# Kernel optimization log

Measured on AMD Instinct MI355X. Metric: run time of the kernel, lower is better.

The kernel has to match this reference:

```python
import jax, jax.numpy as jnp
import numpy as np

T = 2048          # tokens (single causal prefill sequence)
H = 4096          # hidden_size
NH = 32           # num query heads
NKV = 8           # num kv heads (GQA)
HD = H // NH      # head_dim = 128
ROPE_THETA = 500000.0
Q_SIZE = NH * HD
KV_SIZE = NKV * HD


def setup_inputs() -> dict:
    key = jax.random.key(0)
    k1, k2, k3 = jax.random.split(key, 3)
    return {
        "positions": jnp.arange(T, dtype=jnp.int32),
        "hidden_states": jax.random.normal(k1, (T, H), dtype=jnp.float32) * 0.02,
        "w_qkv": jax.random.normal(k2, (H, Q_SIZE + 2 * KV_SIZE), dtype=jnp.float32) * (1.0 / np.sqrt(H)),
        "w_o": jax.random.normal(k3, (Q_SIZE, H), dtype=jnp.float32) * (1.0 / np.sqrt(Q_SIZE)),
    }


def _apply_rope(x, positions):
    # x: [T, heads, HD]; neox-style (non-interleaved) RoPE as in get_rope
    half = HD // 2
    inv_freq = 1.0 / (ROPE_THETA ** (jnp.arange(0, half, dtype=jnp.float32) / half * 1.0))
    # note: standard llama uses arange(0, HD, 2)/HD == arange(half)/half
    freqs = positions.astype(jnp.float32)[:, None] * inv_freq[None, :]   # [T, half]
    cos = jnp.cos(freqs)[:, None, :]  # [T, 1, half]
    sin = jnp.sin(freqs)[:, None, :]
    x1, x2 = x[..., :half], x[..., half:]
    return jnp.concatenate([x1 * cos - x2 * sin, x2 * cos + x1 * sin], axis=-1).astype(x.dtype)


def reference(positions, hidden_states, w_qkv, w_o):
    # qkv_proj (no bias)
    qkv = hidden_states @ w_qkv                               # [T, 6144]
    q, k, v = jnp.split(qkv, [Q_SIZE, Q_SIZE + KV_SIZE], axis=-1)
    q = q.reshape(T, NH, HD)
    k = k.reshape(T, NKV, HD)
    v = v.reshape(T, NKV, HD)

    # fused RoPE on q and k (k would be written rotated into the KV cache)
    q = _apply_rope(q, positions)
    k = _apply_rope(k, positions)

    # GQA: expand kv heads to query heads
    group = NH // NKV
    k_rep = jnp.repeat(k, group, axis=1)                      # [T, NH, HD]
    v_rep = jnp.repeat(v, group, axis=1)

    scale = HD ** -0.5
    scores = jnp.einsum('qhd,shd->hqs', q, k_rep) * scale     # [NH, T, T]
    causal = jnp.tril(jnp.ones((T, T), dtype=bool))
    scores = jnp.where(causal[None], scores, jnp.finfo(scores.dtype).min)
    probs = jax.nn.softmax(scores, axis=-1)
    attn = jnp.einsum('hqs,shd->qhd', probs, v_rep)           # [T, NH, HD]

    out = attn.reshape(T, Q_SIZE) @ w_o                       # o_proj
    return out
```

## Files before the change

### kernel.cpp

```cpp
#include <hip/hip_runtime.h>
#include <cstdint>
#include <cstddef>

#define T_SEQ 2048
#define H_DIM 4096
#define NH 32
#define NKV 8
#define HD 128
#define QKV_N 6144
#define Q_SIZE 4096
#define KV_SIZE 1024

typedef __attribute__((ext_vector_type(8))) short bf16x8;
typedef __attribute__((ext_vector_type(4))) short short4v;
typedef __attribute__((ext_vector_type(4))) float f32x4;

__device__ __forceinline__ short f2bf(float f) {
  union { float f; uint32_t u; } v; v.f = f;
  uint32_t r = v.u + 0x7fffu + ((v.u >> 16) & 1u);
  return (short)(r >> 16);
}

__device__ __forceinline__ void gload_lds16(const void* g, void* l) {
  __builtin_amdgcn_global_load_lds((const __attribute__((address_space(1))) void*)g,
                                   (__attribute__((address_space(3))) void*)l,
                                   16, 0, 0);
}

__global__ __launch_bounds__(256) void cvt_bf16_kernel(const float* __restrict__ in,
                                                       short* __restrict__ out, int n4) {
  int i = blockIdx.x * 256 + threadIdx.x;
  if (i < n4) {
    float4 v = ((const float4*)in)[i];
    short4v s;
    s.x = f2bf(v.x); s.y = f2bf(v.y); s.z = f2bf(v.z); s.w = f2bf(v.w);
    ((short4v*)out)[i] = s;
  }
}

__global__ __launch_bounds__(256) void transpose_cvt_kernel(const float* __restrict__ in,
                                                            short* __restrict__ out,
                                                            int rows, int cols) {
  __shared__ float tile[32][33];
  int bx = blockIdx.x * 32;
  int by = blockIdx.y * 32;
  int x = threadIdx.x, y = threadIdx.y;
#pragma unroll
  for (int i = 0; i < 32; i += 8)
    tile[y + i][x] = in[(size_t)(by + y + i) * cols + bx + x];
  __syncthreads();
#pragma unroll
  for (int i = 0; i < 32; i += 8)
    out[(size_t)(bx + y + i) * rows + by + x] = f2bf(tile[x][y + i]);
}

__global__ __launch_bounds__(256) void gemm_bt_kernel(const short* __restrict__ A,
                                                      const short* __restrict__ Bt,
                                                      float* __restrict__ C,
                                                      int M, int N, int K) {
  __shared__ short As[128 * 32];
  __shared__ short Bs[128 * 32];
  int tid = threadIdx.x;
  int w = tid >> 6, lane = tid & 63;
  int quad = lane >> 4, l16 = lane & 15;
  int wm = (w >> 1) * 64, wn = (w & 1) * 64;
  int bm = blockIdx.y * 128, bn = blockIdx.x * 128;
  f32x4 acc[4][4] = {};
  for (int kk = 0; kk < K; kk += 32) {
    __syncthreads();
#pragma unroll
    for (int p = 0; p < 2; ++p) {
      int e = (p * 256 + tid) * 8;
      int row = e >> 5, kc = e & 31;
      gload_lds16(A + (size_t)(bm + row) * K + kk + kc, As + e);
      gload_lds16(Bt + (size_t)(bn + row) * K + kk + kc, Bs + e);
    }
    __syncthreads();
    bf16x8 af[4], bfr[4];
#pragma unroll
    for (int mi = 0; mi < 4; ++mi)
      af[mi] = *(const bf16x8*)(As + (wm + mi * 16 + l16) * 32 + quad * 8);
#pragma unroll
    for (int ni = 0; ni < 4; ++ni)
      bfr[ni] = *(const bf16x8*)(Bs + (wn + ni * 16 + l16) * 32 + quad * 8);
#pragma unroll
    for (int mi = 0; mi < 4; ++mi)
#pragma unroll
      for (int ni = 0; ni < 4; ++ni)
        acc[mi][ni] = __builtin_amdgcn_mfma_f32_16x16x32_bf16(af[mi], bfr[ni], acc[mi][ni], 0, 0, 0);
  }
#pragma unroll
  for (int mi = 0; mi < 4; ++mi)
#pragma unroll
    for (int ni = 0; ni < 4; ++ni) {
      int r0 = bm + wm + mi * 16 + quad * 4;
      int c0 = bn + wn + ni * 16 + l16;
#pragma unroll
      for (int r = 0; r < 4; ++r)
        C[(size_t)(r0 + r) * N + c0] = acc[mi][ni][r];
    }
}

__global__ __launch_bounds__(256) void rope_kernel(const float* __restrict__ qkv,
                                                   const int* __restrict__ positions,
                                                   short* __restrict__ qb,
                                                   short* __restrict__ kb) {
  int t = blockIdx.x;
  int hh = blockIdx.y * 4 + (threadIdx.x >> 6);
  int j = threadIdx.x & 63;
  float pos = (float)positions[t];
  float f = pos * exp2f(-(float)j * 0.29580575889569017f);
  float c = cosf(f), sn = sinf(f);
  size_t rowbase = (size_t)t * QKV_N;
  int coloff = (hh < NH) ? hh * HD : Q_SIZE + (hh - NH) * HD;
  float x1 = qkv[rowbase + coloff + j];
  float x2 = qkv[rowbase + coloff + j + 64];
  float o1 = x1 * c - x2 * sn;
  float o2 = x2 * c + x1 * sn;
  const float scale2 = 0.08838834764831845f * 1.4426950408889634f;
  short* dst;
  if (hh < NH) {
    o1 *= scale2; o2 *= scale2;
    dst = qb + ((size_t)hh * T_SEQ + t) * HD;
  } else {
    dst = kb + ((size_t)(hh - NH) * T_SEQ + t) * HD;
  }
  dst[j] = f2bf(o1);
  dst[j + 64] = f2bf(o2);
}

__global__ __launch_bounds__(256) void transpose_v_kernel(const float* __restrict__ qkv,
                                                          short* __restrict__ vt) {
  __shared__ float tile[32][33];
  int bx = blockIdx.x * 32;
  int by = blockIdx.y * 32;
  int x = threadIdx.x, y = threadIdx.y;
#pragma unroll
  for (int i = 0; i < 32; i += 8)
    tile[y + i][x] = qkv[(size_t)(by + y + i) * QKV_N + (Q_SIZE + KV_SIZE) + bx + x];
  __syncthreads();
#pragma unroll
  for (int i = 0; i < 32; i += 8)
    vt[(size_t)(bx + y + i) * T_SEQ + by + x] = f2bf(tile[x][y + i]);
}

#define PS_STR 72
__global__ __launch_bounds__(256, 2) void flash_kernel(const short* __restrict__ qb,
                                                       const short* __restrict__ kb,
                                                       const short* __restrict__ vt,
                                                       short* __restrict__ attn) {
  __shared__ short Ks[64 * 128];
  __shared__ short Vs[128 * 64];
  __shared__ short Ps[8][16 * PS_STR];
  int c = (int)gridDim.x - 1 - (int)blockIdx.x;
  int h = blockIdx.y;
  int kvh = h >> 2;
  int tid = threadIdx.x;
  int w = tid >> 6, lane = tid & 63;
  int quad = lane >> 4, l16 = lane & 15;
  int qrow0w = c * 128 + w * 32;

  const short* kbh = kb + (size_t)kvh * T_SEQ * HD;
  const short* vth = vt + (size_t)kvh * HD * T_SEQ;

  bf16x8 qf[2][4];
#pragma unroll
  for (int g = 0; g < 2; ++g) {
    const short* qbase = qb + ((size_t)h * T_SEQ + qrow0w + g * 16 + l16) * HD + quad * 8;
#pragma unroll
    for (int dk = 0; dk < 4; ++dk) qf[g][dk] = *(const bf16x8*)(qbase + dk * 32);
  }
  f32x4 o[2][8] = {};
  float lp[2] = {0.0f, 0.0f};

  int ktmax_blk = 2 * c + 2;
  int ktmax_w = 2 * c + 1 + (w >> 1);

  for (int kt = 0; kt < ktmax_blk; ++kt) {
    int kpos0 = kt * 64;
    __syncthreads();
#pragma unroll
    for (int p4 = 0; p4 < 4; ++p4) {
      int e = p4 * 256 + tid;
      int kr = e >> 4, kp = e & 15;
      gload_lds16(kbh + (size_t)(kpos0 + kr) * HD + ((kp ^ (kr & 7)) * 8), Ks + e * 8);
      int vd = e >> 3, vp = e & 7;
      gload_lds16(vth + (size_t)vd * T_SEQ + kpos0 + ((vp ^ (vd & 7)) * 8), Vs + e * 8);
    }
    __syncthreads();
    if (kt >= ktmax_w) continue;

    f32x4 s[2][4] = {};
#pragma unroll
    for (int mi = 0; mi < 4; ++mi) {
      int kr = mi * 16 + l16;
      const short* kfb = Ks + kr * 128;
      int sw = kr & 7;
#pragma unroll
      for (int dk = 0; dk < 4; ++dk) {
        bf16x8 kf = *(const bf16x8*)(kfb + (((dk * 4 + quad) ^ sw) * 8));
        s[0][mi] = __builtin_amdgcn_mfma_f32_16x16x32_bf16(kf, qf[0][dk], s[0][mi], 0, 0, 0);
        s[1][mi] = __builtin_amdgcn_mfma_f32_16x16x32_bf16(kf, qf[1][dk], s[1][mi], 0, 0, 0);
      }
    }
#pragma unroll
    for (int g = 0; g < 2; ++g) {
      int qr = qrow0w + g * 16 + l16;
      bool need_mask = (kpos0 + 63 > qrow0w + g * 16);
#pragma unroll
      for (int mi = 0; mi < 4; ++mi) {
        float p0, p1, p2, p3;
        if (need_mask) {
          int kp = kpos0 + mi * 16 + quad * 4;
          p0 = exp2f((kp + 0 > qr) ? -1e30f : s[g][mi][0]);
          p1 = exp2f((kp + 1 > qr) ? -1e30f : s[g][mi][1]);
          p2 = exp2f((kp + 2 > qr) ? -1e30f : s[g][mi][2]);
          p3 = exp2f((kp + 3 > qr) ? -1e30f : s[g][mi][3]);
        } else {
          p0 = exp2f(s[g][mi][0]); p1 = exp2f(s[g][mi][1]);
          p2 = exp2f(s[g][mi][2]); p3 = exp2f(s[g][mi][3]);
        }
        lp[g] += p0 + p1 + p2 + p3;
        short4v pk;
        pk.x = f2bf(p0); pk.y = f2bf(p1); pk.z = f2bf(p2); pk.w = f2bf(p3);
        *(short4v*)(&Ps[w * 2 + g][l16 * PS_STR + mi * 16 + quad * 4]) = pk;
      }
    }
#pragma unroll
    for (int kf2 = 0; kf2 < 2; ++kf2) {
      bf16x8 pf0 = *(const bf16x8*)(&Ps[w * 2 + 0][l16 * PS_STR + kf2 * 32 + quad * 8]);
      bf16x8 pf1 = *(const bf16x8*)(&Ps[w * 2 + 1][l16 * PS_STR + kf2 * 32 + quad * 8]);
#pragma unroll
      for (int ni = 0; ni < 8; ++ni) {
        int vd = ni * 16 + l16;
        bf16x8 vf = *(const bf16x8*)(Vs + vd * 64 + (((kf2 * 4 + quad) ^ (vd & 7)) * 8));
        o[0][ni] = __builtin_amdgcn_mfma_f32_16x16x32_bf16(vf, pf0, o[0][ni], 0, 0, 0);
        o[1][ni] = __builtin_amdgcn_mfma_f32_16x16x32_bf16(vf, pf1, o[1][ni], 0, 0, 0);
      }
    }
  }
#pragma unroll
  for (int g = 0; g < 2; ++g) {
    float lt = lp[g];
    lt += __shfl_xor(lt, 16, 64);
    lt += __shfl_xor(lt, 32, 64);
    float rl = 1.0f / lt;
    short* dst = attn + (size_t)(qrow0w + g * 16 + l16) * Q_SIZE + h * HD + quad * 4;
#pragma unroll
    for (int ni = 0; ni < 8; ++ni) {
      short4v ov;
      ov.x = f2bf(o[g][ni][0] * rl); ov.y = f2bf(o[g][ni][1] * rl);
      ov.z = f2bf(o[g][ni][2] * rl); ov.w = f2bf(o[g][ni][3] * rl);
      *(short4v*)(dst + ni * 16) = ov;
    }
  }
}

extern "C" void kernel_launch(void* const* d_in, const int* in_sizes, int n_in,
                              void* d_out, int out_size, void* d_ws, size_t ws_size,
                              hipStream_t stream) {
  const int* positions = (const int*)d_in[0];
  const float* hidden  = (const float*)d_in[1];
  const float* w_qkv   = (const float*)d_in[2];
  const float* w_o     = (const float*)d_in[3];
  float* out = (float*)d_out;

  char* p = (char*)d_ws;
  short* hA    = (short*)p;               short* attn = hA;
  p += (size_t)T_SEQ * H_DIM * 2;
  short* wqkvT = (short*)p;
  p += (size_t)QKV_N * H_DIM * 2;
  float* qkv   = (float*)p;               short* woT = (short*)p;
  short* qb = wqkvT;
  short* kb = qb + (size_t)NH * T_SEQ * HD;
  short* vt = kb + (size_t)NKV * T_SEQ * HD;

  cvt_bf16_kernel<<<dim3(T_SEQ * H_DIM / 4 / 256), 256, 0, stream>>>(hidden, hA, T_SEQ * H_DIM / 4);
  transpose_cvt_kernel<<<dim3(QKV_N / 32, H_DIM / 32), dim3(32, 8), 0, stream>>>(w_qkv, wqkvT, H_DIM, QKV_N);
  gemm_bt_kernel<<<dim3(QKV_N / 128, T_SEQ / 128), 256, 0, stream>>>(hA, wqkvT, qkv, T_SEQ, QKV_N, H_DIM);
  rope_kernel<<<dim3(T_SEQ, (NH + NKV) / 4), 256, 0, stream>>>(qkv, positions, qb, kb);
  transpose_v_kernel<<<dim3(KV_SIZE / 32, T_SEQ / 32), dim3(32, 8), 0, stream>>>(qkv, vt);
  transpose_cvt_kernel<<<dim3(H_DIM / 32, H_DIM / 32), dim3(32, 8), 0, stream>>>(w_o, woT, H_DIM, H_DIM);
  flash_kernel<<<dim3(T_SEQ / 128, NH), 256, 0, stream>>>(qb, kb, vt, attn);
  gemm_bt_kernel<<<dim3(H_DIM / 128, T_SEQ / 128), 256, 0, stream>>>(attn, woT, out, T_SEQ, H_DIM, H_DIM);
}
```

Before: 591.7 us.

## Replace 128x128 GEMM with 256x256 double-buffered, swizzled ping-pong MFMA kernel

Both projection GEMMs now use a new 512-thread kernel with 256x256 output tiles and a 64-wide K step. It double-buffers LDS through async global-to-LDS loads with an XOR swizzle to avoid bank conflicts, and interleaves quarter-tile MFMA batches with staging of the next tiles under barriers and raised wave priority. The aim is more operand reuse per load and hiding global load latency behind matrix math. The cost is far fewer blocks (192 and 128), which can leave many CUs idle on a 256-CU device, plus heavy register and LDS use per block.

```diff
diff --git a/kernel.cpp b/kernel.cpp
--- a/kernel.cpp
+++ b/kernel.cpp
@@ -54,47 +54,143 @@
     out[(size_t)(bx + y + i) * rows + by + x] = f2bf(tile[x][y + i]);
 }
 
-__global__ __launch_bounds__(256) void gemm_bt_kernel(const short* __restrict__ A,
-                                                      const short* __restrict__ Bt,
-                                                      float* __restrict__ C,
-                                                      int M, int N, int K) {
-  __shared__ short As[128 * 32];
-  __shared__ short Bs[128 * 32];
+#define BARRIER() do { __builtin_amdgcn_s_barrier(); \
+                       __builtin_amdgcn_sched_barrier(0); \
+                       asm volatile("" ::: "memory"); } while (0)
+#define VMCNT4() asm volatile("s_waitcnt vmcnt(4)" ::: "memory")
+#define PRIO1 __builtin_amdgcn_s_setprio(1)
+#define PRIO0 __builtin_amdgcn_s_setprio(0)
+
+#define LDA_HALF(BASE, MH) do { \
+  _Pragma("unroll") \
+  for (int m_ = 0; m_ < 4; ++m_) { \
+    _Pragma("unroll") \
+    for (int ks_ = 0; ks_ < 2; ++ks_) { \
+      int row_ = arow + (MH) * 64 + m_ * 16 + l16; \
+      aF[m_][ks_] = *(const bf16x8*)((BASE) + row_ * 64 + (((ks_ * 4 + quad) ^ (row_ & 7)) << 3)); \
+    } } } while (0)
+
+#define LDB_HALF(BASE, NH, DST) do { \
+  _Pragma("unroll") \
+  for (int n_ = 0; n_ < 2; ++n_) { \
+    _Pragma("unroll") \
+    for (int ks_ = 0; ks_ < 2; ++ks_) { \
+      int row_ = brow + (NH) * 32 + n_ * 16 + l16; \
+      (DST)[n_][ks_] = *(const bf16x8*)((BASE) + row_ * 64 + (((ks_ * 4 + quad) ^ (row_ & 7)) << 3)); \
+    } } } while (0)
+
+#define MMQ(MH, NH, BF) do { \
+  _Pragma("unroll") \
+  for (int m_ = 0; m_ < 4; ++m_) { \
+    _Pragma("unroll") \
+    for (int n_ = 0; n_ < 2; ++n_) { \
+      _Pragma("unroll") \
+      for (int ks_ = 0; ks_ < 2; ++ks_) \
+        acc[(MH) * 4 + m_][(NH) * 2 + n_] = __builtin_amdgcn_mfma_f32_16x16x32_bf16( \
+            aF[m_][ks_], (BF)[n_][ks_], acc[(MH) * 4 + m_][(NH) * 2 + n_], 0, 0, 0); \
+    } } } while (0)
+
+__device__ __forceinline__ void stage_half(const short* __restrict__ src, int ldk,
+                                           short* dst, int half, int tid) {
+#pragma unroll
+  for (int q = 0; q < 2; ++q) {
+    int cc = half * 1024 + q * 512 + tid;
+    int row = cc >> 3, cq = cc & 7;
+    gload_lds16(src + (size_t)row * ldk + ((cq ^ (row & 7)) << 3), dst + cc * 8);
+  }
+}
+
+__global__ __launch_bounds__(512, 1) void gemm_bt256_kernel(const short* __restrict__ A,
+                                                            const short* __restrict__ Bt,
+                                                            float* __restrict__ C,
+                                                            int M, int N, int K) {
+  __shared__ short lds[65536];
+  short* As0 = lds;
+  short* Bs0 = lds + 16384;
+  short* As1 = lds + 32768;
+  short* Bs1 = lds + 49152;
   int tid = threadIdx.x;
   int w = tid >> 6, lane = tid & 63;
   int quad = lane >> 4, l16 = lane & 15;
-  int wm = (w >> 1) * 64, wn = (w & 1) * 64;
-  int bm = blockIdx.y * 128, bn = blockIdx.x * 128;
-  f32x4 acc[4][4] = {};
-  for (int kk = 0; kk < K; kk += 32) {
-    __syncthreads();
-#pragma unroll
-    for (int p = 0; p < 2; ++p) {
-      int e = (p * 256 + tid) * 8;
-      int row = e >> 5, kc = e & 31;
-      gload_lds16(A + (size_t)(bm + row) * K + kk + kc, As + e);
-      gload_lds16(Bt + (size_t)(bn + row) * K + kk + kc, Bs + e);
-    }
-    __syncthreads();
-    bf16x8 af[4], bfr[4];
-#pragma unroll
-    for (int mi = 0; mi < 4; ++mi)
-      af[mi] = *(const bf16x8*)(As + (wm + mi * 16 + l16) * 32 + quad * 8);
-#pragma unroll
-    for (int ni = 0; ni < 4; ++ni)
-      bfr[ni] = *(const bf16x8*)(Bs + (wn + ni * 16 + l16) * 32 + quad * 8);
-#pragma unroll
-    for (int mi = 0; mi < 4; ++mi)
-#pragma unroll
-      for (int ni = 0; ni < 4; ++ni)
-        acc[mi][ni] = __builtin_amdgcn_mfma_f32_16x16x32_bf16(af[mi], bfr[ni], acc[mi][ni], 0, 0, 0);
-  }
-#pragma unroll
-  for (int mi = 0; mi < 4; ++mi)
+  int wr = w >> 2, wc = w & 3;
+  int arow = wr * 128, brow = wc * 64;
+  int bm = blockIdx.y * 256, bn = blockIdx.x * 256;
+  const short* Asrc = A + (size_t)bm * K;
+  const short* Bsrc = Bt + (size_t)bn * K;
+  int NT = K >> 6, NI = NT >> 1;
+
+  f32x4 acc[8][4] = {};
+  bf16x8 aF[4][2], b0F[2][2], b1F[2][2];
+
+  stage_half(Asrc, K, As0, 0, tid);
+  stage_half(Asrc, K, As0, 1, tid);
+  stage_half(Bsrc, K, Bs0, 0, tid);
+  stage_half(Bsrc, K, Bs0, 1, tid);
+  stage_half(Bsrc + 64, K, Bs1, 0, tid);
+  stage_half(Bsrc + 64, K, Bs1, 1, tid);
+  VMCNT4();
+  BARRIER();
+
+#pragma unroll 1
+  for (int i = 0; i < NI; ++i) {
+    const short* a1 = Asrc + (size_t)(2 * i + 1) * 64;
+    int kt2 = 2 * i + 2; if (kt2 > NT - 1) kt2 = NT - 1;
+    int kt3 = 2 * i + 3; if (kt3 > NT - 1) kt3 = NT - 1;
+    const short* a2 = Asrc + (size_t)kt2 * 64;
+    const short* b2 = Bsrc + (size_t)kt2 * 64;
+    const short* b3 = Bsrc + (size_t)kt3 * 64;
+
+    LDA_HALF(As0, 0);
+    LDB_HALF(Bs0, 0, b0F);
+    stage_half(a1, K, As1, 0, tid);
+    BARRIER();
+    PRIO1; MMQ(0, 0, b0F); PRIO0;
+    BARRIER();
+    LDB_HALF(Bs0, 1, b1F);
+    stage_half(a1, K, As1, 1, tid);
+    BARRIER();
+    PRIO1; MMQ(0, 1, b1F); PRIO0;
+    BARRIER();
+    LDA_HALF(As0, 1);
+    stage_half(b2, K, Bs0, 0, tid);
+    BARRIER();
+    PRIO1; MMQ(1, 1, b1F); PRIO0;
+    BARRIER();
+    stage_half(b2, K, Bs0, 1, tid);
+    BARRIER();
+    PRIO1; MMQ(1, 0, b0F); PRIO0;
+    VMCNT4();
+    BARRIER();
+    LDA_HALF(As1, 0);
+    LDB_HALF(Bs1, 0, b0F);
+    stage_half(a2, K, As0, 0, tid);
+    BARRIER();
+    PRIO1; MMQ(0, 0, b0F); PRIO0;
+    BARRIER();
+    LDB_HALF(Bs1, 1, b1F);
+    stage_half(a2, K, As0, 1, tid);
+    BARRIER();
+    PRIO1; MMQ(0, 1, b1F); PRIO0;
+    BARRIER();
+    LDA_HALF(As1, 1);
+    stage_half(b3, K, Bs1, 0, tid);
+    BARRIER();
+    PRIO1; MMQ(1, 1, b1F); PRIO0;
+    BARRIER();
+    stage_half(b3, K, Bs1, 1, tid);
+    BARRIER();
+    PRIO1; MMQ(1, 0, b0F); PRIO0;
+    VMCNT4();
+    BARRIER();
+  }
+  asm volatile("s_waitcnt vmcnt(0)" ::: "memory");
+
+#pragma unroll
+  for (int mi = 0; mi < 8; ++mi)
 #pragma unroll
     for (int ni = 0; ni < 4; ++ni) {
-      int r0 = bm + wm + mi * 16 + quad * 4;
-      int c0 = bn + wn + ni * 16 + l16;
+      int r0 = bm + arow + mi * 16 + quad * 4;
+      int c0 = bn + brow + ni * 16 + l16;
 #pragma unroll
       for (int r = 0; r < 4; ++r)
         C[(size_t)(r0 + r) * N + c0] = acc[mi][ni][r];
@@ -277,10 +373,10 @@
 
   cvt_bf16_kernel<<<dim3(T_SEQ * H_DIM / 4 / 256), 256, 0, stream>>>(hidden, hA, T_SEQ * H_DIM / 4);
   transpose_cvt_kernel<<<dim3(QKV_N / 32, H_DIM / 32), dim3(32, 8), 0, stream>>>(w_qkv, wqkvT, H_DIM, QKV_N);
-  gemm_bt_kernel<<<dim3(QKV_N / 128, T_SEQ / 128), 256, 0, stream>>>(hA, wqkvT, qkv, T_SEQ, QKV_N, H_DIM);
+  gemm_bt256_kernel<<<dim3(QKV_N / 256, T_SEQ / 256), 512, 0, stream>>>(hA, wqkvT, qkv, T_SEQ, QKV_N, H_DIM);
   rope_kernel<<<dim3(T_SEQ, (NH + NKV) / 4), 256, 0, stream>>>(qkv, positions, qb, kb);
   transpose_v_kernel<<<dim3(KV_SIZE / 32, T_SEQ / 32), dim3(32, 8), 0, stream>>>(qkv, vt);
   transpose_cvt_kernel<<<dim3(H_DIM / 32, H_DIM / 32), dim3(32, 8), 0, stream>>>(w_o, woT, H_DIM, H_DIM);
   flash_kernel<<<dim3(T_SEQ / 128, NH), 256, 0, stream>>>(qb, kb, vt, attn);
-  gemm_bt_kernel<<<dim3(H_DIM / 128, T_SEQ / 128), 256, 0, stream>>>(attn, woT, out, T_SEQ, H_DIM, H_DIM);
-}
+  gemm_bt256_kernel<<<dim3(H_DIM / 256, T_SEQ / 256), 512, 0, stream>>>(attn, woT, out, T_SEQ, H_DIM, H_DIM);
+}
```

Result: faster. 543.0 us (-8.2%).
